# Kernel tuning notes

Hardware: AMD Instinct MI355X
Metric: run time of the kernel (lower is better)

## Reference

```python
import jax, jax.numpy as jnp
import numpy as np

N_NODES = 100000
N_EDGES = 1600000
DIM_IN = 128
DIM_OUT = 128


def setup_inputs() -> dict:
    key = jax.random.key(0)
    k1, k2, k3 = jax.random.split(key, 3)
    x = jax.random.normal(k1, (N_NODES, DIM_IN), dtype=jnp.float32)
    W = jax.random.normal(k2, (DIM_OUT, DIM_IN), dtype=jnp.float32) * (1.0 / np.sqrt(DIM_IN))
    bias = jnp.zeros((DIM_OUT,), dtype=jnp.float32)
    edge_index = jax.random.randint(k3, (2, N_EDGES), 0, N_NODES, dtype=jnp.int64)
    return {"x": x, "W": W, "bias": bias, "edge_index": edge_index}


def reference(x, W, bias, edge_index):
    N = x.shape[0]
    # add self loops
    loops = jnp.arange(N, dtype=edge_index.dtype)
    row = jnp.concatenate([edge_index[0], loops])  # source nodes (x_j)
    col = jnp.concatenate([edge_index[1], loops])  # target nodes (aggregation)
    # linear transform (no bias inside lin)
    h = x @ W.T  # [N, out]
    # symmetric degree normalization, degree computed over col incl. self loops
    deg = jax.ops.segment_sum(jnp.ones_like(col, dtype=x.dtype), col, num_segments=N)
    deg_inv_sqrt = jnp.where(deg > 0, deg ** -0.5, 0.0)
    norm = deg_inv_sqrt[row] * deg_inv_sqrt[col]  # [E+N]
    # gather-scale-scatter_add
    msg = norm[:, None] * h[row]  # [E+N, out]
    out = jax.ops.segment_sum(msg, col, num_segments=N)
    return out + bias
```

## Files before the change

kernel.cpp:

```cpp
#include <hip/hip_runtime.h>

#define DIM 128
#define CAP 48
#define BUCKET_BLOCKS 1024
#define GEMM_BLOCKS 1568
#define GRID_COMBO (BUCKET_BLOCKS + GEMM_BLOCKS)


typedef __attribute__((ext_vector_type(8))) short bf16x8;
typedef __attribute__((ext_vector_type(4))) float f32x4;
typedef __attribute__((ext_vector_type(4))) int i32x4;

__device__ __forceinline__ unsigned short f2bf(float f) {
  unsigned int u = __float_as_uint(f);
  return (unsigned short)((u + 0x7FFFu + ((u >> 16) & 1u)) >> 16);
}
__device__ __forceinline__ float bf2f(unsigned int s) {
  return __uint_as_float(s << 16);
}
__device__ __forceinline__ void add8(float* a, uint4 v, float s) {
  a[0] += s * bf2f(v.x & 0xFFFF); a[1] += s * bf2f(v.x >> 16);
  a[2] += s * bf2f(v.y & 0xFFFF); a[3] += s * bf2f(v.y >> 16);
  a[4] += s * bf2f(v.z & 0xFFFF); a[5] += s * bf2f(v.z >> 16);
  a[6] += s * bf2f(v.w & 0xFFFF); a[7] += s * bf2f(v.w >> 16);
}

__global__ __launch_bounds__(256) void prep_kernel(
    const float* __restrict__ W, unsigned short* __restrict__ Wb,
    int* __restrict__ cnt, int N) {
  int i = blockIdx.x * 256 + threadIdx.x;
  if (i < DIM * DIM) Wb[i] = f2bf(W[i]);
  if (i < N) cnt[i] = 0;
}

__global__ __launch_bounds__(256) void combo_kernel(
    const int* __restrict__ rows, const int* __restrict__ cols,
    int* __restrict__ cnt, int* __restrict__ csr,
    const float* __restrict__ x, const unsigned short* __restrict__ Wb,
    unsigned short* __restrict__ h, int E, int N) {
  if (blockIdx.x < BUCKET_BLOCKS) {
    int bid = blockIdx.x;
    int g = bid & 7;
    int gblk = bid >> 3;
    int lo = (int)((long long)g * N / 8);
    int hi = (int)((long long)(g + 1) * N / 8);
    const i32x4* cols4 = (const i32x4*)cols;
    const i32x4* rows4 = (const i32x4*)rows;
    int E4 = E >> 2;
    for (int i = gblk * 256 + threadIdx.x; i < E4;
         i += (BUCKET_BLOCKS / 8) * 256) {
      i32x4 c4 = cols4[i];
      bool mx = (c4.x >= lo) & (c4.x < hi);
      bool my = (c4.y >= lo) & (c4.y < hi);
      bool mz = (c4.z >= lo) & (c4.z < hi);
      bool mw = (c4.w >= lo) & (c4.w < hi);
      if (mx | my | mz | mw) {
        i32x4 r4 = rows4[i];
        if (mx) {
          int k = atomicAdd(&cnt[c4.x], 1);
          if (k < CAP) csr[(size_t)c4.x * CAP + k] = r4.x;
        }
        if (my) {
          int k = atomicAdd(&cnt[c4.y], 1);
          if (k < CAP) csr[(size_t)c4.y * CAP + k] = r4.y;
        }
        if (mz) {
          int k = atomicAdd(&cnt[c4.z], 1);
          if (k < CAP) csr[(size_t)c4.z * CAP + k] = r4.z;
        }
        if (mw) {
          int k = atomicAdd(&cnt[c4.w], 1);
          if (k < CAP) csr[(size_t)c4.w * CAP + k] = r4.w;
        }
      }
    }
    if (gblk == 0) {
      for (int e = (E & ~3) + threadIdx.x; e < E; e += 256) {
        int c = cols[e];
        if (c >= lo && c < hi) {
          int k = atomicAdd(&cnt[c], 1);
          if (k < CAP) csr[(size_t)c * CAP + k] = rows[e];
        }
      }
    }
  } else {
    int wid = (blockIdx.x - BUCKET_BLOCKS) * 4 + (threadIdx.x >> 6);
    int m0 = wid * 16;
    if (m0 >= N) return;
    int lane = threadIdx.x & 63;
    int mr = lane & 15;
    int quad = lane >> 4;

    bf16x8 afrag[4];
    const float* xrow = x + (size_t)(m0 + mr) * DIM + quad * 8;
#pragma unroll
    for (int ks = 0; ks < 4; ++ks) {
      float4 lo = *(const float4*)(xrow + ks * 32);
      float4 hi = *(const float4*)(xrow + ks * 32 + 4);
      bf16x8 a;
      a[0] = (short)f2bf(lo.x); a[1] = (short)f2bf(lo.y);
      a[2] = (short)f2bf(lo.z); a[3] = (short)f2bf(lo.w);
      a[4] = (short)f2bf(hi.x); a[5] = (short)f2bf(hi.y);
      a[6] = (short)f2bf(hi.z); a[7] = (short)f2bf(hi.w);
      afrag[ks] = a;
    }

#pragma unroll
    for (int nt = 0; nt < 8; ++nt) {
      f32x4 c = {0.f, 0.f, 0.f, 0.f};
#pragma unroll
      for (int ks = 0; ks < 4; ++ks) {
        bf16x8 b = *(const bf16x8*)(Wb + (size_t)(nt * 16 + mr) * DIM +
                                    ks * 32 + quad * 8);
        c = __builtin_amdgcn_mfma_f32_16x16x32_bf16(afrag[ks], b, c, 0, 0, 0);
      }
#pragma unroll
      for (int r = 0; r < 4; ++r) {
        h[(size_t)(m0 + quad * 4 + r) * DIM + nt * 16 + mr] = f2bf(c[r]);
      }
    }
  }
}

__global__ __launch_bounds__(256) void gather_kernel(
    const uint4* __restrict__ h4, const int* __restrict__ csr,
    const int* __restrict__ cnt, const float4* __restrict__ bias4,
    float* __restrict__ out, int N) {
  int node = blockIdx.x * 16 + (threadIdx.x >> 4);
  if (node >= N) return;
  int lane = threadIdx.x & 15;

  int degN = cnt[node];
  float dn = rsqrtf((float)degN + 1.0f);
  int deg = degN > CAP ? CAP : degN;
  const int* seg = csr + (size_t)node * CAP;

  float acc[8];
  {
    uint4 s = h4[(size_t)node * 16 + lane];
    acc[0] = dn * bf2f(s.x & 0xFFFF); acc[1] = dn * bf2f(s.x >> 16);
    acc[2] = dn * bf2f(s.y & 0xFFFF); acc[3] = dn * bf2f(s.y >> 16);
    acc[4] = dn * bf2f(s.z & 0xFFFF); acc[5] = dn * bf2f(s.z >> 16);
    acc[6] = dn * bf2f(s.w & 0xFFFF); acc[7] = dn * bf2f(s.w >> 16);
  }
  int j = 0;
  for (; j + 8 <= deg; j += 8) {
    i32x4 ra = __builtin_nontemporal_load((const i32x4*)(seg + j));
    i32x4 rb = __builtin_nontemporal_load((const i32x4*)(seg + j + 4));
    uint4 v0 = h4[(size_t)ra.x * 16 + lane];
    uint4 v1 = h4[(size_t)ra.y * 16 + lane];
    uint4 v2 = h4[(size_t)ra.z * 16 + lane];
    uint4 v3 = h4[(size_t)ra.w * 16 + lane];
    uint4 v4 = h4[(size_t)rb.x * 16 + lane];
    uint4 v5 = h4[(size_t)rb.y * 16 + lane];
    uint4 v6 = h4[(size_t)rb.z * 16 + lane];
    uint4 v7 = h4[(size_t)rb.w * 16 + lane];
    float d0 = rsqrtf((float)cnt[ra.x] + 1.0f);
    float d1 = rsqrtf((float)cnt[ra.y] + 1.0f);
    float d2 = rsqrtf((float)cnt[ra.z] + 1.0f);
    float d3 = rsqrtf((float)cnt[ra.w] + 1.0f);
    float d4 = rsqrtf((float)cnt[rb.x] + 1.0f);
    float d5 = rsqrtf((float)cnt[rb.y] + 1.0f);
    float d6 = rsqrtf((float)cnt[rb.z] + 1.0f);
    float d7 = rsqrtf((float)cnt[rb.w] + 1.0f);
    add8(acc, v0, d0); add8(acc, v1, d1);
    add8(acc, v2, d2); add8(acc, v3, d3);
    add8(acc, v4, d4); add8(acc, v5, d5);
    add8(acc, v6, d6); add8(acc, v7, d7);
  }
  if (j + 4 <= deg) {
    i32x4 r4 = __builtin_nontemporal_load((const i32x4*)(seg + j));
    uint4 v0 = h4[(size_t)r4.x * 16 + lane];
    uint4 v1 = h4[(size_t)r4.y * 16 + lane];
    uint4 v2 = h4[(size_t)r4.z * 16 + lane];
    uint4 v3 = h4[(size_t)r4.w * 16 + lane];
    float d0 = rsqrtf((float)cnt[r4.x] + 1.0f);
    float d1 = rsqrtf((float)cnt[r4.y] + 1.0f);
    float d2 = rsqrtf((float)cnt[r4.z] + 1.0f);
    float d3 = rsqrtf((float)cnt[r4.w] + 1.0f);
    add8(acc, v0, d0); add8(acc, v1, d1);
    add8(acc, v2, d2); add8(acc, v3, d3);
    j += 4;
  }
  for (; j < deg; ++j) {
    int r = __builtin_nontemporal_load(seg + j);
    uint4 v = h4[(size_t)r * 16 + lane];
    float dr = rsqrtf((float)cnt[r] + 1.0f);
    add8(acc, v, dr);
  }
  float4 bA = bias4[lane * 2], bB = bias4[lane * 2 + 1];
  f32x4 oA = {dn * acc[0] + bA.x, dn * acc[1] + bA.y,
              dn * acc[2] + bA.z, dn * acc[3] + bA.w};
  f32x4 oB = {dn * acc[4] + bB.x, dn * acc[5] + bB.y,
              dn * acc[6] + bB.z, dn * acc[7] + bB.w};
  f32x4* outv = (f32x4*)out;
  __builtin_nontemporal_store(oA, &outv[(size_t)node * 32 + lane * 2]);
  __builtin_nontemporal_store(oB, &outv[(size_t)node * 32 + lane * 2 + 1]);
}

extern "C" void kernel_launch(void* const* d_in, const int* in_sizes, int n_in,
                              void* d_out, int out_size, void* d_ws, size_t ws_size,
                              hipStream_t stream) {
  const float* x    = (const float*)d_in[0];
  const float* W    = (const float*)d_in[1];
  const float* bias = (const float*)d_in[2];
  const int*   ei   = (const int*)d_in[3];

  const int N = in_sizes[0] / DIM;
  const int E = in_sizes[3] / 2;
  const int* rows = ei;
  const int* cols = ei + E;
  float* out = (float*)d_out;
  char* ws = (char*)d_ws;

  int* cnt = (int*)ws;
  unsigned short* Wb = (unsigned short*)(ws + 409600);
  int* csr = (int*)(ws + 442368);
  unsigned short* h = (unsigned short*)(ws + 19642368);

  prep_kernel<<<(N + 255) / 256, 256, 0, stream>>>(W, Wb, cnt, N);
  combo_kernel<<<GRID_COMBO, 256, 0, stream>>>(rows, cols, cnt, csr, x, Wb, h,
                                               E, N);
  gather_kernel<<<(N + 15) / 16, 256, 0, stream>>>(
      (const uint4*)h, csr, cnt, (const float4*)bias, (float*)out, N);
}
```

Measured before the change: 265.5 us.

## Replace global-atomic CSR build with two-level bucket sort via shared-memory histograms

Swaps the per-node global atomicAdd bucketing for a counting sort. Edges are first histogrammed into 32-node buckets per block in shared memory, then scanned and scattered into a bucket-partitioned edge array. A per-bucket build kernel then fills the per-node CSR slots using shared-memory atomics. This is meant to remove global atomic contention and scattered writes, at the cost of two extra kernel launches and an extra pass over the edge list.

```diff
diff --git a/kernel.cpp b/kernel.cpp
--- a/kernel.cpp
+++ b/kernel.cpp
@@ -2,9 +2,11 @@
 
 #define DIM 128
 #define CAP 48
-#define BUCKET_BLOCKS 1024
-#define GEMM_BLOCKS 1568
-#define GRID_COMBO (BUCKET_BLOCKS + GEMM_BLOCKS)
+#define NPB 32
+#define NBUK_MAX 3200
+#define NA 128
+#define SCAN_BLOCKS 13
+#define GEMM_BLOCKS 1563
 
 
 typedef __attribute__((ext_vector_type(8))) short bf16x8;
@@ -25,100 +27,171 @@
   a[6] += s * bf2f(v.w & 0xFFFF); a[7] += s * bf2f(v.w >> 16);
 }
 
-__global__ __launch_bounds__(256) void prep_kernel(
+__global__ __launch_bounds__(256) void prepA_kernel(
     const float* __restrict__ W, unsigned short* __restrict__ Wb,
-    int* __restrict__ cnt, int N) {
-  int i = blockIdx.x * 256 + threadIdx.x;
-  if (i < DIM * DIM) Wb[i] = f2bf(W[i]);
-  if (i < N) cnt[i] = 0;
+    const int* __restrict__ cols, int* __restrict__ ghist, int E, int nbuk) {
+  int bid = blockIdx.x;
+  if (bid >= NA) {
+    int i = (bid - NA) * 256 + threadIdx.x;
+    if (i < DIM * DIM) Wb[i] = f2bf(W[i]);
+    return;
+  }
+  __shared__ int hist[NBUK_MAX];
+  for (int t = threadIdx.x; t < nbuk; t += 256) hist[t] = 0;
+  __syncthreads();
+  int E4 = E >> 2;
+  int ce4 = (E4 + NA - 1) / NA;
+  int beg = bid * ce4, end = min(beg + ce4, E4);
+  const i32x4* cols4 = (const i32x4*)cols;
+  for (int i = beg + threadIdx.x; i < end; i += 256) {
+    i32x4 c4 = cols4[i];
+    atomicAdd(&hist[c4.x >> 5], 1);
+    atomicAdd(&hist[c4.y >> 5], 1);
+    atomicAdd(&hist[c4.z >> 5], 1);
+    atomicAdd(&hist[c4.w >> 5], 1);
+  }
+  if (bid == NA - 1) {
+    for (int e = (E & ~3) + threadIdx.x; e < E; e += 256)
+      atomicAdd(&hist[cols[e] >> 5], 1);
+  }
+  __syncthreads();
+  for (int t = threadIdx.x; t < nbuk; t += 256)
+    ghist[(size_t)t * NA + bid] = hist[t];
 }
 
 __global__ __launch_bounds__(256) void combo_kernel(
-    const int* __restrict__ rows, const int* __restrict__ cols,
-    int* __restrict__ cnt, int* __restrict__ csr,
+    int* __restrict__ ghist, int* __restrict__ tot,
     const float* __restrict__ x, const unsigned short* __restrict__ Wb,
-    unsigned short* __restrict__ h, int E, int N) {
-  if (blockIdx.x < BUCKET_BLOCKS) {
-    int bid = blockIdx.x;
-    int g = bid & 7;
-    int gblk = bid >> 3;
-    int lo = (int)((long long)g * N / 8);
-    int hi = (int)((long long)(g + 1) * N / 8);
-    const i32x4* cols4 = (const i32x4*)cols;
-    const i32x4* rows4 = (const i32x4*)rows;
-    int E4 = E >> 2;
-    for (int i = gblk * 256 + threadIdx.x; i < E4;
-         i += (BUCKET_BLOCKS / 8) * 256) {
-      i32x4 c4 = cols4[i];
-      bool mx = (c4.x >= lo) & (c4.x < hi);
-      bool my = (c4.y >= lo) & (c4.y < hi);
-      bool mz = (c4.z >= lo) & (c4.z < hi);
-      bool mw = (c4.w >= lo) & (c4.w < hi);
-      if (mx | my | mz | mw) {
-        i32x4 r4 = rows4[i];
-        if (mx) {
-          int k = atomicAdd(&cnt[c4.x], 1);
-          if (k < CAP) csr[(size_t)c4.x * CAP + k] = r4.x;
-        }
-        if (my) {
-          int k = atomicAdd(&cnt[c4.y], 1);
-          if (k < CAP) csr[(size_t)c4.y * CAP + k] = r4.y;
-        }
-        if (mz) {
-          int k = atomicAdd(&cnt[c4.z], 1);
-          if (k < CAP) csr[(size_t)c4.z * CAP + k] = r4.z;
-        }
-        if (mw) {
-          int k = atomicAdd(&cnt[c4.w], 1);
-          if (k < CAP) csr[(size_t)c4.w * CAP + k] = r4.w;
-        }
+    unsigned short* __restrict__ h, int N, int nbuk) {
+  if (blockIdx.x < SCAN_BLOCKS) {
+    int g = blockIdx.x * 256 + threadIdx.x;
+    if (g < nbuk) {
+      int* row = ghist + (size_t)g * NA;
+      int run = 0;
+      for (int b = 0; b < NA; ++b) {
+        int v = row[b]; row[b] = run; run += v;
       }
+      tot[g] = run;
     }
-    if (gblk == 0) {
-      for (int e = (E & ~3) + threadIdx.x; e < E; e += 256) {
-        int c = cols[e];
-        if (c >= lo && c < hi) {
-          int k = atomicAdd(&cnt[c], 1);
-          if (k < CAP) csr[(size_t)c * CAP + k] = rows[e];
-        }
-      }
-    }
-  } else {
-    int wid = (blockIdx.x - BUCKET_BLOCKS) * 4 + (threadIdx.x >> 6);
-    int m0 = wid * 16;
-    if (m0 >= N) return;
-    int lane = threadIdx.x & 63;
-    int mr = lane & 15;
-    int quad = lane >> 4;
-
-    bf16x8 afrag[4];
-    const float* xrow = x + (size_t)(m0 + mr) * DIM + quad * 8;
+    return;
+  }
+  int wid = (blockIdx.x - SCAN_BLOCKS) * 4 + (threadIdx.x >> 6);
+  int m0 = wid * 16;
+  if (m0 >= N) return;
+  int lane = threadIdx.x & 63;
+  int mr = lane & 15;
+  int quad = lane >> 4;
+
+  bf16x8 afrag[4];
+  const float* xrow = x + (size_t)(m0 + mr) * DIM + quad * 8;
+#pragma unroll
+  for (int ks = 0; ks < 4; ++ks) {
+    float4 lo = *(const float4*)(xrow + ks * 32);
+    float4 hi = *(const float4*)(xrow + ks * 32 + 4);
+    bf16x8 a;
+    a[0] = (short)f2bf(lo.x); a[1] = (short)f2bf(lo.y);
+    a[2] = (short)f2bf(lo.z); a[3] = (short)f2bf(lo.w);
+    a[4] = (short)f2bf(hi.x); a[5] = (short)f2bf(hi.y);
+    a[6] = (short)f2bf(hi.z); a[7] = (short)f2bf(hi.w);
+    afrag[ks] = a;
+  }
+#pragma unroll
+  for (int nt = 0; nt < 8; ++nt) {
+    f32x4 c = {0.f, 0.f, 0.f, 0.f};
 #pragma unroll
     for (int ks = 0; ks < 4; ++ks) {
-      float4 lo = *(const float4*)(xrow + ks * 32);
-      float4 hi = *(const float4*)(xrow + ks * 32 + 4);
-      bf16x8 a;
-      a[0] = (short)f2bf(lo.x); a[1] = (short)f2bf(lo.y);
-      a[2] = (short)f2bf(lo.z); a[3] = (short)f2bf(lo.w);
-      a[4] = (short)f2bf(hi.x); a[5] = (short)f2bf(hi.y);
-      a[6] = (short)f2bf(hi.z); a[7] = (short)f2bf(hi.w);
-      afrag[ks] = a;
+      bf16x8 b = *(const bf16x8*)(Wb + (size_t)(nt * 16 + mr) * DIM +
+                                  ks * 32 + quad * 8);
+      c = __builtin_amdgcn_mfma_f32_16x16x32_bf16(afrag[ks], b, c, 0, 0, 0);
     }
-
 #pragma unroll
-    for (int nt = 0; nt < 8; ++nt) {
-      f32x4 c = {0.f, 0.f, 0.f, 0.f};
-#pragma unroll
-      for (int ks = 0; ks < 4; ++ks) {
-        bf16x8 b = *(const bf16x8*)(Wb + (size_t)(nt * 16 + mr) * DIM +
-                                    ks * 32 + quad * 8);
-        c = __builtin_amdgcn_mfma_f32_16x16x32_bf16(afrag[ks], b, c, 0, 0, 0);
-      }
-#pragma unroll
-      for (int r = 0; r < 4; ++r) {
-        h[(size_t)(m0 + quad * 4 + r) * DIM + nt * 16 + mr] = f2bf(c[r]);
-      }
+    for (int r = 0; r < 4; ++r) {
+      h[(size_t)(m0 + quad * 4 + r) * DIM + nt * 16 + mr] = f2bf(c[r]);
     }
+  }
+}
+
+__global__ __launch_bounds__(256) void scatter_kernel(
+    const int* __restrict__ rows, const int* __restrict__ cols,
+    const int* __restrict__ ghist, const int* __restrict__ tot,
+    int* __restrict__ basebuf, unsigned int* __restrict__ epart,
+    int E, int nbuk) {
+  __shared__ int sB[NBUK_MAX];
+  __shared__ int sPart[256];
+  int tid = threadIdx.x, bid = blockIdx.x;
+  for (int t = tid; t < nbuk; t += 256) sB[t] = tot[t];
+  __syncthreads();
+  int cpt = (nbuk + 255) / 256;
+  int b0 = tid * cpt, b1 = min(b0 + cpt, nbuk);
+  int s = 0;
+  for (int i = b0; i < b1; ++i) s += sB[i];
+  sPart[tid] = s;
+  __syncthreads();
+  if (tid == 0) {
+    int run = 0;
+    for (int i = 0; i < 256; ++i) { int v = sPart[i]; sPart[i] = run; run += v; }
+  }
+  __syncthreads();
+  {
+    int run = sPart[tid];
+    for (int i = b0; i < b1; ++i) { int v = sB[i]; sB[i] = run; run += v; }
+  }
+  __syncthreads();
+  if (bid == 0) {
+    for (int t = tid; t < nbuk; t += 256) basebuf[t] = sB[t];
+    if (tid == 0) basebuf[nbuk] = E;
+  }
+  for (int t = tid; t < nbuk; t += 256) sB[t] += ghist[(size_t)t * NA + bid];
+  __syncthreads();
+  int E4 = E >> 2;
+  int ce4 = (E4 + NA - 1) / NA;
+  int beg = bid * ce4, end = min(beg + ce4, E4);
+  const i32x4* cols4 = (const i32x4*)cols;
+  const i32x4* rows4 = (const i32x4*)rows;
+  for (int i = beg + tid; i < end; i += 256) {
+    i32x4 c4 = cols4[i];
+    i32x4 r4 = rows4[i];
+    int k;
+    k = atomicAdd(&sB[c4.x >> 5], 1);
+    epart[k] = ((unsigned)r4.x << 5) | (unsigned)(c4.x & 31);
+    k = atomicAdd(&sB[c4.y >> 5], 1);
+    epart[k] = ((unsigned)r4.y << 5) | (unsigned)(c4.y & 31);
+    k = atomicAdd(&sB[c4.z >> 5], 1);
+    epart[k] = ((unsigned)r4.z << 5) | (unsigned)(c4.z & 31);
+    k = atomicAdd(&sB[c4.w >> 5], 1);
+    epart[k] = ((unsigned)r4.w << 5) | (unsigned)(c4.w & 31);
+  }
+  if (bid == NA - 1) {
+    for (int e = (E & ~3) + tid; e < E; e += 256) {
+      int c = cols[e];
+      int k = atomicAdd(&sB[c >> 5], 1);
+      epart[k] = ((unsigned)rows[e] << 5) | (unsigned)(c & 31);
+    }
+  }
+}
+
+__global__ __launch_bounds__(256) void build_kernel(
+    const unsigned int* __restrict__ epart, const int* __restrict__ basebuf,
+    int* __restrict__ cnt, int* __restrict__ csr, int N) {
+  int g = blockIdx.x;
+  __shared__ int lcnt[NPB];
+  __shared__ int lcsr[NPB * CAP];
+  int tid = threadIdx.x;
+  if (tid < NPB) lcnt[tid] = 0;
+  __syncthreads();
+  int beg = basebuf[g], end = basebuf[g + 1];
+  for (int e = beg + tid; e < end; e += 256) {
+    unsigned v = epart[e];
+    int c = (int)(v & 31);
+    int r = (int)(v >> 5);
+    int k = atomicAdd(&lcnt[c], 1);
+    if (k < CAP) lcsr[c * CAP + k] = r;
+  }
+  __syncthreads();
+  int node0 = g * NPB;
+  if (tid < NPB && node0 + tid < N) cnt[node0 + tid] = lcnt[tid];
+  for (int t = tid; t < NPB * CAP; t += 256) {
+    if (node0 + t / CAP < N) csr[(size_t)node0 * CAP + t] = lcsr[t];
   }
 }
 
@@ -212,15 +285,23 @@
   const int* cols = ei + E;
   float* out = (float*)d_out;
   char* ws = (char*)d_ws;
+  const int nbuk = (N + NPB - 1) / NPB;
 
   int* cnt = (int*)ws;
-  unsigned short* Wb = (unsigned short*)(ws + 409600);
-  int* csr = (int*)(ws + 442368);
-  unsigned short* h = (unsigned short*)(ws + 19642368);
-
-  prep_kernel<<<(N + 255) / 256, 256, 0, stream>>>(W, Wb, cnt, N);
-  combo_kernel<<<GRID_COMBO, 256, 0, stream>>>(rows, cols, cnt, csr, x, Wb, h,
-                                               E, N);
+  int* tot = (int*)(ws + 400000);
+  int* basebuf = (int*)(ws + 412512);
+  unsigned short* Wb = (unsigned short*)(ws + 425024);
+  int* ghist = (int*)(ws + 457792);
+  unsigned int* epart = (unsigned int*)(ws + 2057792);
+  int* csr = (int*)(ws + 8457792);
+  unsigned short* h = (unsigned short*)(ws + 27657792);
+
+  prepA_kernel<<<NA + 64, 256, 0, stream>>>(W, Wb, cols, ghist, E, nbuk);
+  combo_kernel<<<SCAN_BLOCKS + GEMM_BLOCKS, 256, 0, stream>>>(
+      ghist, tot, x, Wb, h, N, nbuk);
+  scatter_kernel<<<NA, 256, 0, stream>>>(rows, cols, ghist, tot, basebuf,
+                                         epart, E, nbuk);
+  build_kernel<<<nbuk, 256, 0, stream>>>(epart, basebuf, cnt, csr, N);
   gather_kernel<<<(N + 15) / 16, 256, 0, stream>>>(
       (const uint4*)h, csr, cnt, (const float4*)bias, (float*)out, N);
 }
```

Measured after the change: 288.2 us. 8.6% more time.
